# Optimization experiments

Hardware: AMD Instinct MI355X
Metric: run time of the kernel (lower is better)

Reference implementation:

```python
import jax, jax.numpy as jnp
import numpy as np

# irreps multiplicities: node = NSx0e + NVx1o, edge = ESx0e + EVx1o, hidden = HSx0e + HVx1o
NS, NV = 64, 32
ES, EV = 8, 8
HS, HV = 96, 32          # Gate splits HS scalars -> (HS-HV) silu scalars + HV sigmoid gates
N_NODES, N_EDGES = 10000, 100000
INV_SQRT3 = float(1.0 / np.sqrt(3.0))  # w3j(1,1,0) coefficient


def _split(x, ns, nv):
    # [N, ns + 3*nv] -> scalars [N, ns], vectors [N, nv, 3]
    return x[:, :ns], x[:, ns:].reshape(x.shape[0], nv, 3)


def _merge(s, v):
    return jnp.concatenate([s, v.reshape(v.shape[0], -1)], axis=-1)


def _fc_tp(xs, xv, ys, yv, w_ss, w_vv, w_sv, w_vs):
    """FullyConnectedTensorProduct for l<=1 irreps with path ('element') normalization.
    Paths: 0e*0e->0e, 1o*1o->0e (dot/sqrt3), 0e*1o->1o, 1o*0e->1o."""
    fan_s = w_ss.shape[0] * w_ss.shape[1] + w_vv.shape[0] * w_vv.shape[1]
    fan_v = w_sv.shape[0] * w_sv.shape[1] + w_vs.shape[0] * w_vs.shape[1]
    out_s = (jnp.einsum('eu,ev,uvw->ew', xs, ys, w_ss)
             + INV_SQRT3 * jnp.einsum('eum,evm,uvw->ew', xv, yv, w_vv)) / np.sqrt(fan_s)
    out_v = (jnp.einsum('eu,evm,uvw->ewm', xs, yv, w_sv)
             + jnp.einsum('eum,ev,uvw->ewm', xv, ys, w_vs)) / np.sqrt(fan_v)
    return out_s, out_v


def _gate(s, v, n_plain):
    # e3nn Gate: silu on plain scalars, sigmoid gates multiply each vector channel
    plain = jax.nn.silu(s[:, :n_plain])
    gates = jax.nn.sigmoid(s[:, n_plain:])
    return plain, v * gates[:, :, None]


def _lin(s, v, Ws, Wv):
    # e3nn equivariant Linear: mixes multiplicities per irrep, shared over m, 1/sqrt(fan_in)
    return (s @ Ws) / np.sqrt(Ws.shape[0]), jnp.einsum('num,uw->nwm', v, Wv) / np.sqrt(Wv.shape[0])


def setup_inputs() -> dict:
    key = jax.random.key(0)
    ks = jax.random.split(key, 15)
    rn = lambda k, sh: jax.random.normal(k, sh, dtype=jnp.float32)
    return {
        'node_features': rn(ks[0], (N_NODES, NS + 3 * NV)),
        'edge_attr': rn(ks[1], (N_EDGES, ES + 3 * EV)),
        'w_msg_ss': rn(ks[2], (NS, ES, HS)),
        'w_msg_vv': rn(ks[3], (NV, EV, HS)),
        'w_msg_sv': rn(ks[4], (NS, EV, HV)),
        'w_msg_vs': rn(ks[5], (NV, ES, HV)),
        'w_lin_msg_s': rn(ks[6], (HS - HV, HS)),
        'w_lin_msg_v': rn(ks[7], (HV, HV)),
        'w_upd_ss': rn(ks[8], (NS, HS, HS)),
        'w_upd_vv': rn(ks[9], (NV, HV, HS)),
        'w_upd_sv': rn(ks[10], (NS, HV, HV)),
        'w_upd_vs': rn(ks[11], (NV, HS, HV)),
        'w_lin_upd_s': rn(ks[12], (HS - HV, NS)),
        'w_lin_upd_v': rn(ks[13], (HV, NV)),
        'edge_index': jax.random.randint(ks[14], (2, N_EDGES), 0, N_NODES),
    }


def reference(node_features, edge_attr, w_msg_ss, w_msg_vv, w_msg_sv, w_msg_vs,
              w_lin_msg_s, w_lin_msg_v, w_upd_ss, w_upd_vv, w_upd_sv, w_upd_vs,
              w_lin_upd_s, w_lin_upd_v, edge_index):
    row, col = edge_index[0], edge_index[1]
    ns, nv = _split(node_features, NS, NV)
    es, ev = _split(edge_attr, ES, EV)

    # messages: gather -> CG tensor product -> gate -> linear
    ms, mv = _fc_tp(ns[col], nv[col], es, ev, w_msg_ss, w_msg_vv, w_msg_sv, w_msg_vs)
    ps, pv = _gate(ms, mv, HS - HV)                  # [E, HS-HV], [E, HV, 3]
    ls, lv = _lin(ps, pv, w_lin_msg_s, w_lin_msg_v)  # [E, HS],    [E, HV, 3]

    # scatter-sum aggregation onto destination nodes
    agg_s = jax.ops.segment_sum(ls, row, num_segments=N_NODES)
    agg_v = jax.ops.segment_sum(lv, row, num_segments=N_NODES)

    # node update: CG tensor product with aggregated messages -> gate -> linear -> residual
    us, uv = _fc_tp(ns, nv, agg_s, agg_v, w_upd_ss, w_upd_vv, w_upd_sv, w_upd_vs)
    gs, gv = _gate(us, uv, HS - HV)
    ds, dv = _lin(gs, gv, w_lin_upd_s, w_lin_upd_v)  # [N, NS], [N, NV, 3]
    return _merge(ns + ds, nv + dv)
```

## Files before the change

### kernel.cpp

```cpp
#include <hip/hip_runtime.h>
#include <hip/hip_bf16.h>

constexpr int kNodes = 10000;
constexpr int kEdges = 100000;

constexpr float INV_SQRT3    = 0.57735026918962576f;
constexpr float INV_SQRT768  = 0.036084391824351615f;
constexpr float INV_SQRT7168 = 0.011811389781538352f;
constexpr float INV_SQRT5120 = 0.013975424859373686f;
constexpr float INV_SQRT32   = 0.17677669529663687f;

constexpr size_t MSGW_OFF  = 0;
constexpr size_t UPDW1_OFF = 196608;
constexpr size_t UPDW2_OFF = 1572864;
constexpr size_t MLINS_OFF = 1900544;
constexpr size_t MLINV_OFF = 1912832;
constexpr size_t ULINS_OFF = 1914880;
constexpr size_t ULINV_OFF = 1923072;

typedef __attribute__((ext_vector_type(8))) short bf8;
typedef __attribute__((ext_vector_type(4))) float f4;
union BF { bf8 v; short s[8]; unsigned u[4]; };

__device__ __forceinline__ short f2bf(float f) {
    union { float f; unsigned u; } c; c.f = f;
    unsigned r = c.u + 0x7fffu + ((c.u >> 16) & 1u);
    return (short)(r >> 16);
}
__device__ __forceinline__ unsigned pk2(float lo, float hi) {
    union { __hip_bfloat162 h; unsigned u; } c;
    c.h = __float22bfloat162_rn(make_float2(lo, hi));
    return c.u;
}
__device__ __forceinline__ f4 mfma16(bf8 a, bf8 b, f4 c) {
    return __builtin_amdgcn_mfma_f32_16x16x32_bf16(a, b, c, 0, 0, 0);
}
__device__ __forceinline__ bf8 ldB(const char* p) {
    return *(const bf8*)p;
}
__device__ __forceinline__ float fsig(float x) { return 1.0f / (1.0f + __expf(-x)); }

__global__ void prep_kernel(
    const float* __restrict__ Wmss, const float* __restrict__ Wmvv,
    const float* __restrict__ Wmsv, const float* __restrict__ Wmvs,
    const float* __restrict__ Wlms, const float* __restrict__ Wlmv,
    const float* __restrict__ Wuss, const float* __restrict__ Wuvv,
    const float* __restrict__ Wusv, const float* __restrict__ Wuvs,
    const float* __restrict__ Wlus, const float* __restrict__ Wluv,
    char* __restrict__ wout)
{
    int i = blockIdx.x * 256 + threadIdx.x;
    float v;
    short* dst;
    if (i < 98304) {
        dst = (short*)(wout + MSGW_OFF) + i;
        int t = i >> 12, q = i & 4095, r = q >> 5, c = q & 31;
        int k = t * 32 + c;
        if (r < 96) {
            v = (k < 512 ? Wmss[k * 96 + r]
                         : Wmvv[(k - 512) * 96 + r] * INV_SQRT3) * INV_SQRT768;
        } else {
            int n2 = r - 96;
            if (k < 512) { int u = k & 63, vv = k >> 6; v = Wmsv[(u * 8 + vv) * 32 + n2] * INV_SQRT768; }
            else         { v = Wmvs[(k - 512) * 32 + n2] * INV_SQRT768; }
        }
    } else if (i < 786432) {
        int j = i - 98304;
        dst = (short*)(wout + UPDW1_OFF) + j;
        int t = j / 3072, q = j % 3072, r = q >> 5, c = q & 31;
        int k = t * 32 + c;
        if (k < 6144) { int u = k & 63, vv = k >> 6;
            v = Wuss[(u * 96 + vv) * 96 + r] * INV_SQRT7168; }
        else { int r2 = k - 6144; int u = r2 & 31, vv = r2 >> 5;
            v = Wuvv[(u * 32 + vv) * 96 + r] * (INV_SQRT3 * INV_SQRT7168); }
    } else if (i < 950272) {
        int j = i - 786432;
        dst = (short*)(wout + UPDW2_OFF) + j;
        int t = j >> 10, q = j & 1023, r = q >> 5, c = q & 31;
        int k = t * 32 + c;
        if (k < 2048) { int u = k & 63, vv = k >> 6;
            v = Wusv[(u * 32 + vv) * 32 + r] * INV_SQRT5120; }
        else { int r2 = k - 2048;
            v = Wuvs[r2 * 32 + r] * INV_SQRT5120; }
    } else if (i < 956416) {
        int j = i - 950272;
        dst = (short*)(wout + MLINS_OFF) + j;
        int n = j >> 6, kk = j & 63;
        v = Wlms[kk * 96 + n] * 0.125f;
    } else if (i < 957440) {
        int j = i - 956416;
        dst = (short*)(wout + MLINV_OFF) + j;
        int n = j >> 5, kk = j & 31;
        v = Wlmv[kk * 32 + n] * INV_SQRT32;
    } else if (i < 961536) {
        int j = i - 957440;
        dst = (short*)(wout + ULINS_OFF) + j;
        int n = j >> 6, kk = j & 63;
        v = Wlus[kk * 64 + n] * 0.125f;
    } else if (i < 962560) {
        int j = i - 961536;
        dst = (short*)(wout + ULINV_OFF) + j;
        int n = j >> 5, kk = j & 31;
        v = Wluv[kk * 32 + n] * INV_SQRT32;
    } else return;
    *dst = f2bf(v);
}

__global__ __launch_bounds__(256, 3) void msg_kernel(
    const float* __restrict__ nf, const float* __restrict__ ea,
    const int* __restrict__ eidx, const char* __restrict__ wout,
    float* __restrict__ agg)
{
    __shared__ float nf_sh[32 * 164];
    __shared__ float ea_sh[32 * 36];
    __shared__ int   row_sh[32];
    __shared__ float gat[32 * 36];
    __shared__ short silu_s[32 * 72];
    __shared__ short pv_s[96 * 40];

    const int t = threadIdx.x, w = t >> 6, lane = t & 63;
    const int l15 = lane & 15, lg = lane >> 4;
    const int eblk = blockIdx.x * 32;

    const char* msgW = wout + MSGW_OFF;

    {
        const int i = t >> 3, j = t & 7;
        const int e = eblk + i;
        if (j == 0) row_sh[i] = eidx[e];
        const int col = eidx[kEdges + e];
        const float4* src = (const float4*)(nf + (size_t)col * 160);
        for (int c = j; c < 40; c += 8) *(float4*)&nf_sh[i * 164 + c * 4] = src[c];
        const float4* esrc = (const float4*)(ea + (size_t)e * 32);
        *(float4*)&ea_sh[i * 36 + j * 4] = esrc[j];
    }
    __syncthreads();

    f4 accS[3] = {{0.f,0.f,0.f,0.f},{0.f,0.f,0.f,0.f},{0.f,0.f,0.f,0.f}};
    f4 accV[3] = {{0.f,0.f,0.f,0.f},{0.f,0.f,0.f,0.f},{0.f,0.f,0.f,0.f}};
    const int Ms = w >> 1, nb = (w & 1) * 3;
    const int es_ = Ms * 16 + l15;

    const float4 ey0 = *(const float4*)&ea_sh[es_ * 36];
    const float4 ey1 = *(const float4*)&ea_sh[es_ * 36 + 4];
    float eyv[24];
    #pragma unroll
    for (int q = 0; q < 6; ++q)
        *(float4*)&eyv[q * 4] = *(const float4*)&ea_sh[es_ * 36 + 8 + q * 4];

    for (int kt = 0; kt < 16; ++kt) {
        const char* wb = msgW + kt * 8192;
        BF aS;
        {
            const int uu = kt * 4 + lg;
            const float xs = nf_sh[es_ * 164 + uu];
            aS.u[0] = pk2(xs * ey0.x, xs * ey0.y);
            aS.u[1] = pk2(xs * ey0.z, xs * ey0.w);
            aS.u[2] = pk2(xs * ey1.x, xs * ey1.y);
            aS.u[3] = pk2(xs * ey1.z, xs * ey1.w);
        }
        #pragma unroll
        for (int i = 0; i < 3; ++i)
            accS[i] = mfma16(aS.v, ldB(wb + ((nb + i) * 16 + l15) * 64 + lg * 16), accS[i]);

        BF aV; int prevMv = -1;
        #pragma unroll
        for (int i = 0; i < 3; ++i) {
            const int tv = 3 * w + i, Mv = tv >> 1, Nv = tv & 1;
            if (Mv != prevMv) {
                prevMv = Mv;
                const int m = Mv >> 1, ev = (Mv & 1) * 16 + l15;
                const int kp = kt * 32 + lg * 8;
                const int vv = kp >> 6, u0 = kp & 63;
                const float ym = ea_sh[ev * 36 + 8 + 3 * vv + m];
                const float4 x0 = *(const float4*)&nf_sh[ev * 164 + u0];
                const float4 x1 = *(const float4*)&nf_sh[ev * 164 + u0 + 4];
                aV.u[0] = pk2(x0.x * ym, x0.y * ym);
                aV.u[1] = pk2(x0.z * ym, x0.w * ym);
                aV.u[2] = pk2(x1.x * ym, x1.y * ym);
                aV.u[3] = pk2(x1.z * ym, x1.w * ym);
            }
            accV[i] = mfma16(aV.v, ldB(wb + (96 + (Nv * 16 + l15)) * 64 + lg * 16), accV[i]);
        }
    }
    for (int kt = 16; kt < 24; ++kt) {
        const char* wb = msgW + kt * 8192;
        BF aS;
        {
            const int uu = (kt - 16) * 4 + lg;
            const float* xp = &nf_sh[es_ * 164 + 64 + 3 * uu];
            const float x0 = xp[0], x1 = xp[1], x2 = xp[2];
            #pragma unroll
            for (int j = 0; j < 4; ++j) {
                float a0 = x0 * eyv[6*j  ] + x1 * eyv[6*j+1] + x2 * eyv[6*j+2];
                float a1 = x0 * eyv[6*j+3] + x1 * eyv[6*j+4] + x2 * eyv[6*j+5];
                aS.u[j] = pk2(a0, a1);
            }
        }
        #pragma unroll
        for (int i = 0; i < 3; ++i)
            accS[i] = mfma16(aS.v, ldB(wb + ((nb + i) * 16 + l15) * 64 + lg * 16), accS[i]);

        BF aV; int prevMv = -1;
        #pragma unroll
        for (int i = 0; i < 3; ++i) {
            const int tv = 3 * w + i, Mv = tv >> 1, Nv = tv & 1;
            if (Mv != prevMv) {
                prevMv = Mv;
                const int m = Mv >> 1, ev = (Mv & 1) * 16 + l15;
                const int uu = (kt - 16) * 4 + lg;
                const float xm = nf_sh[ev * 164 + 64 + 3 * uu + m];
                const float4 y0 = *(const float4*)&ea_sh[ev * 36];
                const float4 y1 = *(const float4*)&ea_sh[ev * 36 + 4];
                aV.u[0] = pk2(xm * y0.x, xm * y0.y);
                aV.u[1] = pk2(xm * y0.z, xm * y0.w);
                aV.u[2] = pk2(xm * y1.x, xm * y1.y);
                aV.u[3] = pk2(xm * y1.z, xm * y1.w);
            }
            accV[i] = mfma16(aV.v, ldB(wb + (96 + (Nv * 16 + l15)) * 64 + lg * 16), accV[i]);
        }
    }

    #pragma unroll
    for (int i = 0; i < 3; ++i) {
        const int n = (nb + i) * 16 + l15;
        #pragma unroll
        for (int r = 0; r < 4; ++r) {
            const int e = Ms * 16 + lg * 4 + r;
            const float v = accS[i][r];
            if (n < 64) silu_s[e * 72 + n] = f2bf(v * fsig(v));
            else        gat[e * 36 + (n - 64)] = fsig(v);
        }
    }
    __syncthreads();
    #pragma unroll
    for (int i = 0; i < 3; ++i) {
        const int tv = 3 * w + i, Mv = tv >> 1, Nv = tv & 1;
        const int m = Mv >> 1, eb = (Mv & 1) * 16;
        const int u = Nv * 16 + l15;
        #pragma unroll
        for (int r = 0; r < 4; ++r) {
            const int e = eb + lg * 4 + r;
            pv_s[(m * 32 + e) * 40 + u] = f2bf(accV[i][r] * gat[e * 36 + u]);
        }
    }
    __syncthreads();

    {
        const char* mls = wout + MLINS_OFF;
        f4 acc[3] = {{0.f,0.f,0.f,0.f},{0.f,0.f,0.f,0.f},{0.f,0.f,0.f,0.f}};
        #pragma unroll
        for (int k0 = 0; k0 < 2; ++k0) {
            const int kg = k0 * 32 + lg * 8;
            bf8 a = *(const bf8*)&silu_s[es_ * 72 + kg];
            #pragma unroll
            for (int i = 0; i < 3; ++i)
                acc[i] = mfma16(a, ldB(mls + ((nb + i) * 16 + l15) * 128 + kg * 2), acc[i]);
        }
        #pragma unroll
        for (int i = 0; i < 3; ++i) {
            const int n = (nb + i) * 16 + l15;
            #pragma unroll
            for (int r = 0; r < 4; ++r) {
                const int e = Ms * 16 + lg * 4 + r;
                atomicAdd(&agg[(size_t)row_sh[e] * 192 + n], acc[i][r]);
            }
        }
    }
    {
        const char* mlv = wout + MLINV_OFF;
        f4 acc[3] = {{0.f,0.f,0.f,0.f},{0.f,0.f,0.f,0.f},{0.f,0.f,0.f,0.f}};
        const int kg = lg * 8;
        BF a; int prevMv = -1;
        #pragma unroll
        for (int i = 0; i < 3; ++i) {
            const int tv = 3 * w + i, Mv = tv >> 1, Nv = tv & 1;
            if (Mv != prevMv) { prevMv = Mv; a.v = *(const bf8*)&pv_s[(Mv * 16 + l15) * 40 + kg]; }
            acc[i] = mfma16(a.v, ldB(mlv + (Nv * 16 + l15) * 64 + kg * 2), acc[i]);
        }
        #pragma unroll
        for (int i = 0; i < 3; ++i) {
            const int tv = 3 * w + i, Mv = tv >> 1, Nv = tv & 1;
            const int w2 = Nv * 16 + l15;
            #pragma unroll
            for (int r = 0; r < 4; ++r) {
                const int rr = Mv * 16 + lg * 4 + r;
                const int m = rr >> 5, e = rr & 31;
                atomicAdd(&agg[(size_t)row_sh[e] * 192 + 96 + w2 * 3 + m], acc[i][r]);
            }
        }
    }
}

__global__ __launch_bounds__(512, 4) void upd_kernel(
    const float* __restrict__ nf, const char* __restrict__ wout,
    float* __restrict__ agg)
{
    __shared__ float nf_sh[32 * 164];
    __shared__ float ag_sh[32 * 196];
    __shared__ float gat[32 * 36];
    __shared__ short silu_s[32 * 72];
    __shared__ short gv_s[96 * 40];
    __shared__ float red[3072];

    const int t = threadIdx.x, w = t >> 6, lane = t & 63;
    const int g = w >> 2, wl = w & 3;
    const int l15 = lane & 15, lg = lane >> 4;
    const int nblk = blockIdx.x * 32;
    const char* W1 = wout + UPDW1_OFF;
    const char* W2 = wout + UPDW2_OFF;

    {
        const int i = t >> 4, j = t & 15;
        int n = nblk + i; if (n > kNodes - 1) n = kNodes - 1;
        const float4* src = (const float4*)(nf + (size_t)n * 160);
        for (int c = j; c < 40; c += 16) *(float4*)&nf_sh[i * 164 + c * 4] = src[c];
        const float4* asrc = (const float4*)(agg + (size_t)n * 192);
        for (int c = j; c < 48; c += 16) *(float4*)&ag_sh[i * 196 + c * 4] = asrc[c];
    }
    __syncthreads();

    const int Ms = wl >> 1, nb = (wl & 1) * 3;
    const int es_ = Ms * 16 + l15;

    f4 accS[3] = {{0.f,0.f,0.f,0.f},{0.f,0.f,0.f,0.f},{0.f,0.f,0.f,0.f}};
    {
        const int kt0 = g * 112, kt1 = kt0 + 112;
        const int ktSS = kt1 < 192 ? kt1 : 192;
        int kt = kt0;
        for (; kt < ktSS; ++kt) {
            const char* wb = W1 + (size_t)kt * 6144;
            const int kp = kt * 32 + lg * 8;
            const int vv = kp >> 6, u0 = kp & 63;
            const float ys = ag_sh[es_ * 196 + vv];
            const float4 x0 = *(const float4*)&nf_sh[es_ * 164 + u0];
            const float4 x1 = *(const float4*)&nf_sh[es_ * 164 + u0 + 4];
            BF aS;
            aS.u[0] = pk2(x0.x * ys, x0.y * ys);
            aS.u[1] = pk2(x0.z * ys, x0.w * ys);
            aS.u[2] = pk2(x1.x * ys, x1.y * ys);
            aS.u[3] = pk2(x1.z * ys, x1.w * ys);
            #pragma unroll
            for (int i = 0; i < 3; ++i)
                accS[i] = mfma16(aS.v, ldB(wb + ((nb + i) * 16 + l15) * 64 + lg * 16), accS[i]);
        }
        for (; kt < kt1; ++kt) {
            const char* wb = W1 + (size_t)kt * 6144;
            const int rp = kt * 32 + lg * 8 - 6144;
            const int vv = rp >> 5, u0 = rp & 31;
            const float* xp = &nf_sh[es_ * 164 + 64 + 3 * u0];
            const float* gp = &ag_sh[es_ * 196 + 96 + 3 * vv];
            const float g0 = gp[0], g1 = gp[1], g2 = gp[2];
            BF aS;
            #pragma unroll
            for (int j = 0; j < 4; ++j) {
                float a0 = xp[6*j  ] * g0 + xp[6*j+1] * g1 + xp[6*j+2] * g2;
                float a1 = xp[6*j+3] * g0 + xp[6*j+4] * g1 + xp[6*j+5] * g2;
                aS.u[j] = pk2(a0, a1);
            }
            #pragma unroll
            for (int i = 0; i < 3; ++i)
                accS[i] = mfma16(aS.v, ldB(wb + ((nb + i) * 16 + l15) * 64 + lg * 16), accS[i]);
        }
    }

    if (g == 1) {
        #pragma unroll
        for (int i = 0; i < 3; ++i) {
            const int n = (nb + i) * 16 + l15;
            #pragma unroll
            for (int r = 0; r < 4; ++r)
                red[(Ms * 16 + lg * 4 + r) * 96 + n] = accS[i][r];
        }
    }
    __syncthreads();
    if (g == 0) {
        #pragma unroll
        for (int i = 0; i < 3; ++i) {
            const int n = (nb + i) * 16 + l15;
            #pragma unroll
            for (int r = 0; r < 4; ++r) {
                const int e = Ms * 16 + lg * 4 + r;
                const float v = accS[i][r] + red[e * 96 + n];
                if (n < 64) silu_s[e * 72 + n] = f2bf(v * fsig(v));
                else        gat[e * 36 + (n - 64)] = fsig(v);
            }
        }
    }
    __syncthreads();

    f4 accV[3] = {{0.f,0.f,0.f,0.f},{0.f,0.f,0.f,0.f},{0.f,0.f,0.f,0.f}};
    {
        const int kt0 = g * 80, kt1 = kt0 + 80;
        const int ktSV = kt1 < 64 ? kt1 : 64;
        int kt = kt0;
        for (; kt < ktSV; ++kt) {
            const char* wb = W2 + (size_t)kt * 2048;
            BF aV; int prevMv = -1;
            #pragma unroll
            for (int i = 0; i < 3; ++i) {
                const int tv = 3 * wl + i, Mv = tv >> 1, Nv = tv & 1;
                if (Mv != prevMv) {
                    prevMv = Mv;
                    const int m = Mv >> 1, ev = (Mv & 1) * 16 + l15;
                    const int kp = kt * 32 + lg * 8;
                    const int vv = kp >> 6, u0 = kp & 63;
                    const float ym = ag_sh[ev * 196 + 96 + 3 * vv + m];
                    const float4 x0 = *(const float4*)&nf_sh[ev * 164 + u0];
                    const float4 x1 = *(const float4*)&nf_sh[ev * 164 + u0 + 4];
                    aV.u[0] = pk2(x0.x * ym, x0.y * ym);
                    aV.u[1] = pk2(x0.z * ym, x0.w * ym);
                    aV.u[2] = pk2(x1.x * ym, x1.y * ym);
                    aV.u[3] = pk2(x1.z * ym, x1.w * ym);
                }
                accV[i] = mfma16(aV.v, ldB(wb + (Nv * 16 + l15) * 64 + lg * 16), accV[i]);
            }
        }
        for (; kt < kt1; ++kt) {
            const char* wb = W2 + (size_t)kt * 2048;
            BF aV; int prevMv = -1;
            #pragma unroll
            for (int i = 0; i < 3; ++i) {
                const int tv = 3 * wl + i, Mv = tv >> 1, Nv = tv & 1;
                if (Mv != prevMv) {
                    prevMv = Mv;
                    const int m = Mv >> 1, ev = (Mv & 1) * 16 + l15;
                    const int rp = kt * 32 + lg * 8 - 2048;
                    const int u = rp / 96, v0 = rp - u * 96;
                    const float xm = nf_sh[ev * 164 + 64 + 3 * u + m];
                    const float4 y0 = *(const float4*)&ag_sh[ev * 196 + v0];
                    const float4 y1 = *(const float4*)&ag_sh[ev * 196 + v0 + 4];
                    aV.u[0] = pk2(xm * y0.x, xm * y0.y);
                    aV.u[1] = pk2(xm * y0.z, xm * y0.w);
                    aV.u[2] = pk2(xm * y1.x, xm * y1.y);
                    aV.u[3] = pk2(xm * y1.z, xm * y1.w);
                }
                accV[i] = mfma16(aV.v, ldB(wb + (Nv * 16 + l15) * 64 + lg * 16), accV[i]);
            }
        }
    }

    if (g == 1) {
        #pragma unroll
        for (int i = 0; i < 3; ++i) {
            const int tv = 3 * wl + i, Mv = tv >> 1, Nv = tv & 1;
            #pragma unroll
            for (int r = 0; r < 4; ++r)
                red[(Mv * 16 + lg * 4 + r) * 32 + Nv * 16 + l15] = accV[i][r];
        }
    }
    __syncthreads();
    if (g == 0) {
        #pragma unroll
        for (int i = 0; i < 3; ++i) {
            const int tv = 3 * wl + i, Mv = tv >> 1, Nv = tv & 1;
            const int m = Mv >> 1, eb = (Mv & 1) * 16;
            const int u = Nv * 16 + l15;
            #pragma unroll
            for (int r = 0; r < 4; ++r) {
                const int e = eb + lg * 4 + r;
                const float v = accV[i][r] + red[(Mv * 16 + lg * 4 + r) * 32 + u];
                gv_s[(m * 32 + e) * 40 + u] = f2bf(v * gat[e * 36 + u]);
            }
        }
    }
    __syncthreads();

    const int nvalid = kNodes - nblk;
    if (g == 0) {
        {
            const char* uls = wout + ULINS_OFF;
            f4 acc[2] = {{0.f,0.f,0.f,0.f},{0.f,0.f,0.f,0.f}};
            const int nb2 = (wl & 1) * 2;
            #pragma unroll
            for (int k0 = 0; k0 < 2; ++k0) {
                const int kg = k0 * 32 + lg * 8;
                bf8 a = *(const bf8*)&silu_s[es_ * 72 + kg];
                #pragma unroll
                for (int i = 0; i < 2; ++i)
                    acc[i] = mfma16(a, ldB(uls + ((nb2 + i) * 16 + l15) * 128 + kg * 2), acc[i]);
            }
            #pragma unroll
            for (int i = 0; i < 2; ++i) {
                const int n = (nb2 + i) * 16 + l15;
                #pragma unroll
                for (int r = 0; r < 4; ++r) {
                    const int e = Ms * 16 + lg * 4 + r;
                    if (e < nvalid)
                        agg[(size_t)(nblk + e) * 192 + n] = nf_sh[e * 164 + n] + acc[i][r];
                }
            }
        }
        {
            const char* ulv = wout + ULINV_OFF;
            f4 acc[3] = {{0.f,0.f,0.f,0.f},{0.f,0.f,0.f,0.f},{0.f,0.f,0.f,0.f}};
            const int kg = lg * 8;
            BF a; int prevMv = -1;
            #pragma unroll
            for (int i = 0; i < 3; ++i) {
                const int tv = 3 * wl + i, Mv = tv >> 1, Nv = tv & 1;
                if (Mv != prevMv) { prevMv = Mv; a.v = *(const bf8*)&gv_s[(Mv * 16 + l15) * 40 + kg]; }
                acc[i] = mfma16(a.v, ldB(ulv + (Nv * 16 + l15) * 64 + kg * 2), acc[i]);
            }
            #pragma unroll
            for (int i = 0; i < 3; ++i) {
                const int tv = 3 * wl + i, Mv = tv >> 1, Nv = tv & 1;
                const int w2 = Nv * 16 + l15;
                #pragma unroll
                for (int r = 0; r < 4; ++r) {
                    const int rr = Mv * 16 + lg * 4 + r;
                    const int m = rr >> 5, e = rr & 31;
                    if (e < nvalid)
                        agg[(size_t)(nblk + e) * 192 + 64 + w2 * 3 + m]
                            = nf_sh[e * 164 + 64 + w2 * 3 + m] + acc[i][r];
                }
            }
        }
    }
}

__global__ __launch_bounds__(256) void copy_kernel(const float* __restrict__ agg,
                                                   float* __restrict__ out)
{
    int i = blockIdx.x * 256 + threadIdx.x;
    if (i < 400000) {
        int n = i / 40, c = i - n * 40;
        ((float4*)out)[i] = ((const float4*)agg)[n * 48 + c];
    }
}

extern "C" void kernel_launch(void* const* d_in, const int* in_sizes, int n_in,
                              void* d_out, int out_size, void* d_ws, size_t ws_size,
                              hipStream_t stream) {
    const float* nf   = (const float*)d_in[0];
    const float* ea   = (const float*)d_in[1];
    const int*   eidx = (const int*)d_in[14];
    float* agg = (float*)d_ws;
    char*  wout = (char*)d_out;

    hipMemsetAsync(agg, 0, 7680000, stream);
    prep_kernel<<<3760, 256, 0, stream>>>(
        (const float*)d_in[2], (const float*)d_in[3], (const float*)d_in[4],
        (const float*)d_in[5], (const float*)d_in[6], (const float*)d_in[7],
        (const float*)d_in[8], (const float*)d_in[9], (const float*)d_in[10],
        (const float*)d_in[11], (const float*)d_in[12], (const float*)d_in[13], wout);
    msg_kernel<<<kEdges / 32, 256, 0, stream>>>(nf, ea, eidx, wout, agg);
    upd_kernel<<<(kNodes + 31) / 32, 512, 0, stream>>>(nf, wout, agg);
    copy_kernel<<<1563, 256, 0, stream>>>(agg, (float*)d_out);
}
```

Measured before the change: 463.3 us.

## Sort edges by destination and pre-reduce messages in shared memory before global atomics

Adds histogram, single-block scan and scatter kernels that build a permutation grouping edges by destination node. The message kernel then processes edges in that order and accumulates each block's outputs into a shared-memory buffer keyed by the first edge with the same destination. Only one global atomic per distinct destination and channel is issued. The aim is to cut global atomic traffic. In exchange it adds three small launches, one of them a serial single-block scan, plus an extra memset, reuses LDS through aliasing, and the scatter order of edges within a node is nondeterministic.

```diff
diff --git a/kernel.cpp b/kernel.cpp
--- a/kernel.cpp
+++ b/kernel.cpp
@@ -17,6 +17,9 @@
 constexpr size_t MLINV_OFF = 1912832;
 constexpr size_t ULINS_OFF = 1914880;
 constexpr size_t ULINV_OFF = 1923072;
+constexpr size_t CNT_OFF   = 1926144;
+constexpr size_t CUR_OFF   = 1967104;
+constexpr size_t PERM_OFF  = 2008064;
 
 typedef __attribute__((ext_vector_type(8))) short bf8;
 typedef __attribute__((ext_vector_type(4))) float f4;
@@ -106,32 +109,72 @@
     *dst = f2bf(v);
 }
 
+__global__ __launch_bounds__(256) void hist_kernel(const int* __restrict__ eidx,
+                                                   int* __restrict__ cnt)
+{
+    int e = blockIdx.x * 256 + threadIdx.x;
+    if (e < kEdges) atomicAdd(&cnt[eidx[e]], 1);
+}
+
+__global__ __launch_bounds__(256) void scan_kernel(const int* __restrict__ cnt,
+                                                   int* __restrict__ cursor)
+{
+    __shared__ int psum[256];
+    const int t = threadIdx.x, base = t * 40;
+    int s = 0;
+    for (int j = 0; j < 40; ++j) { int idx = base + j; if (idx < kNodes) s += cnt[idx]; }
+    psum[t] = s;
+    __syncthreads();
+    if (t == 0) { int a = 0; for (int i = 0; i < 256; ++i) { int x = psum[i]; psum[i] = a; a += x; } }
+    __syncthreads();
+    int run = psum[t];
+    for (int j = 0; j < 40; ++j) {
+        int idx = base + j;
+        if (idx < kNodes) { cursor[idx] = run; run += cnt[idx]; }
+    }
+}
+
+__global__ __launch_bounds__(256) void scatter_kernel(const int* __restrict__ eidx,
+                                                      int* __restrict__ cursor,
+                                                      int* __restrict__ perm)
+{
+    int e = blockIdx.x * 256 + threadIdx.x;
+    if (e < kEdges) {
+        int p = atomicAdd(&cursor[eidx[e]], 1);
+        perm[p] = e;
+    }
+}
+
 __global__ __launch_bounds__(256, 3) void msg_kernel(
     const float* __restrict__ nf, const float* __restrict__ ea,
     const int* __restrict__ eidx, const char* __restrict__ wout,
     float* __restrict__ agg)
 {
-    __shared__ float nf_sh[32 * 164];
-    __shared__ float ea_sh[32 * 36];
-    __shared__ int   row_sh[32];
-    __shared__ float gat[32 * 36];
-    __shared__ short silu_s[32 * 72];
-    __shared__ short pv_s[96 * 40];
+    __shared__ char pool[42752];
+    float* nf_sh   = (float*)pool;
+    float* ea_sh   = (float*)(pool + 20992);
+    float* aggloc  = (float*)pool;
+    int*   row_sh  = (int*)  (pool + 25600);
+    int*   rank_sh = (int*)  (pool + 25728);
+    float* gat     = (float*)(pool + 25856);
+    short* silu_s  = (short*)(pool + 30464);
+    short* pv_s    = (short*)(pool + 35072);
 
     const int t = threadIdx.x, w = t >> 6, lane = t & 63;
     const int l15 = lane & 15, lg = lane >> 4;
     const int eblk = blockIdx.x * 32;
 
     const char* msgW = wout + MSGW_OFF;
+    const int*  perm = (const int*)(wout + PERM_OFF);
 
     {
         const int i = t >> 3, j = t & 7;
-        const int e = eblk + i;
-        if (j == 0) row_sh[i] = eidx[e];
-        const int col = eidx[kEdges + e];
+        const int pe = perm[eblk + i];
+        if (j == 0) row_sh[i] = eidx[pe];
+        const int col = eidx[kEdges + pe];
         const float4* src = (const float4*)(nf + (size_t)col * 160);
         for (int c = j; c < 40; c += 8) *(float4*)&nf_sh[i * 164 + c * 4] = src[c];
-        const float4* esrc = (const float4*)(ea + (size_t)e * 32);
+        const float4* esrc = (const float4*)(ea + (size_t)pe * 32);
         *(float4*)&ea_sh[i * 36 + j * 4] = esrc[j];
     }
     __syncthreads();
@@ -221,6 +264,8 @@
         }
     }
 
+    __syncthreads();
+
     #pragma unroll
     for (int i = 0; i < 3; ++i) {
         const int n = (nb + i) * 16 + l15;
@@ -232,7 +277,15 @@
             else        gat[e * 36 + (n - 64)] = fsig(v);
         }
     }
-    __syncthreads();
+    for (int idx = t; idx < 32 * 192; idx += 256) aggloc[idx] = 0.f;
+    if (t < 32) {
+        const int ri = row_sh[t];
+        int rk = t;
+        for (int j2 = 0; j2 < t; ++j2) if (row_sh[j2] == ri) { rk = j2; break; }
+        rank_sh[t] = rk;
+    }
+    __syncthreads();
+
     #pragma unroll
     for (int i = 0; i < 3; ++i) {
         const int tv = 3 * w + i, Mv = tv >> 1, Nv = tv & 1;
@@ -263,7 +316,7 @@
             #pragma unroll
             for (int r = 0; r < 4; ++r) {
                 const int e = Ms * 16 + lg * 4 + r;
-                atomicAdd(&agg[(size_t)row_sh[e] * 192 + n], acc[i][r]);
+                atomicAdd(&aggloc[rank_sh[e] * 192 + n], acc[i][r]);
             }
         }
     }
@@ -286,9 +339,16 @@
             for (int r = 0; r < 4; ++r) {
                 const int rr = Mv * 16 + lg * 4 + r;
                 const int m = rr >> 5, e = rr & 31;
-                atomicAdd(&agg[(size_t)row_sh[e] * 192 + 96 + w2 * 3 + m], acc[i][r]);
-            }
-        }
+                atomicAdd(&aggloc[rank_sh[e] * 192 + 96 + w2 * 3 + m], acc[i][r]);
+            }
+        }
+    }
+    __syncthreads();
+
+    for (int idx = t; idx < 32 * 192; idx += 256) {
+        const int ii = idx / 192, c = idx - ii * 192;
+        if (rank_sh[ii] == ii)
+            atomicAdd(&agg[(size_t)row_sh[ii] * 192 + c], aggloc[idx]);
     }
 }
 
@@ -539,11 +599,15 @@
     char*  wout = (char*)d_out;
 
     hipMemsetAsync(agg, 0, 7680000, stream);
+    hipMemsetAsync(wout + CNT_OFF, 0, 40960, stream);
     prep_kernel<<<3760, 256, 0, stream>>>(
         (const float*)d_in[2], (const float*)d_in[3], (const float*)d_in[4],
         (const float*)d_in[5], (const float*)d_in[6], (const float*)d_in[7],
         (const float*)d_in[8], (const float*)d_in[9], (const float*)d_in[10],
         (const float*)d_in[11], (const float*)d_in[12], (const float*)d_in[13], wout);
+    hist_kernel<<<391, 256, 0, stream>>>(eidx, (int*)(wout + CNT_OFF));
+    scan_kernel<<<1, 256, 0, stream>>>((const int*)(wout + CNT_OFF), (int*)(wout + CUR_OFF));
+    scatter_kernel<<<391, 256, 0, stream>>>(eidx, (int*)(wout + CUR_OFF), (int*)(wout + PERM_OFF));
     msg_kernel<<<kEdges / 32, 256, 0, stream>>>(nf, ea, eidx, wout, agg);
     upd_kernel<<<(kNodes + 31) / 32, 512, 0, stream>>>(nf, wout, agg);
     copy_kernel<<<1563, 256, 0, stream>>>(agg, (float*)d_out);
```

New measurement: 524.9 us. 1.13x slower.
